# Kernel optimization log

Hardware: AMD Instinct MI355X
Metric: run time of the kernel (lower is better)

Reference implementation:

```python
import jax, jax.numpy as jnp
import numpy as np

D = 128  # time-encoder dimension == attention embed_dim


def harmonic_encode(ts, basis_freq):
    # ts: (N,) -> (N, D); phases are zero in the original module
    m = ts[:, None] * basis_freq[None, :]
    return jnp.sqrt(1.0 / D) * jnp.concatenate([jnp.cos(m), jnp.sin(m)], axis=1)


def mha_1head(q, k, mask, Wq, bq, Wk, bk, Wv, bv, Wo, bo):
    # Single-head nn.MultiheadAttention. q: (T, D) queries (torch batch dim),
    # k: (S, D) shared keys/values (original repeats these T times; same math),
    # mask: (T, S) True = masked out (key_padding_mask semantics).
    qp = q @ Wq.T + bq
    kp = k @ Wk.T + bk
    vp = k @ Wv.T + bv
    scores = jnp.einsum('td,sd->ts', qp, kp) / jnp.sqrt(jnp.asarray(D, q.dtype))
    scores = jnp.where(mask, -jnp.inf, scores)
    attn = jax.nn.softmax(scores, axis=-1)  # (T, S)
    return (attn @ vp) @ Wo.T + bo


def setup_inputs() -> dict:
    key = jax.random.key(0)
    ks = jax.random.split(key, 24)
    T, L, V = 4096, 8192, 1000
    s = 1.0 / np.sqrt(D)
    inp = {
        't': jax.random.uniform(ks[0], (T,), jnp.float32),
        'e_nodes_ts': jax.random.uniform(ks[1], (L,), jnp.float32),
        'e_nodes_exp': jax.random.randint(ks[2], (L,), 0, V),
        'e_node_target': jax.random.randint(ks[3], (1,), 0, V),
        'basis_freq': jnp.asarray(1.0 / 5.0 ** np.linspace(1, 9, D // 2), jnp.float32),
        'phi': jnp.ones((1,), jnp.float32),
        'W_lin': jax.random.normal(ks[4], (1, 2 * D), jnp.float32) * 0.05,
        'b_lin': jnp.zeros((1,), jnp.float32),
    }
    kidx = 5
    for suf in ('_s', '_n'):
        for nm in ('Wq', 'Wk', 'Wv', 'Wo'):
            inp[nm + suf] = jax.random.normal(ks[kidx], (D, D), jnp.float32) * s
            kidx += 1
        for nm in ('bq', 'bk', 'bv', 'bo'):
            inp[nm + suf] = jnp.zeros((D,), jnp.float32)
    return inp


def reference(t, e_nodes_ts, e_nodes_exp, e_node_target, basis_freq, phi, W_lin, b_lin,
              Wq_s, Wk_s, Wv_s, Wo_s, bq_s, bk_s, bv_s, bo_s,
              Wq_n, Wk_n, Wv_n, Wo_n, bq_n, bk_n, bv_n, bo_n):
    # prepend sentinels exactly as the torch forward does
    ts_all = jnp.concatenate([jnp.zeros((2,), e_nodes_ts.dtype), e_nodes_ts])      # (S,)
    exp_all = jnp.concatenate([jnp.full((1,), -1, e_nodes_exp.dtype), e_node_target, e_nodes_exp])  # (S,)

    phi_t = harmonic_encode(t, basis_freq)        # (T, D)
    phi_ts = harmonic_encode(ts_all, basis_freq)  # (S, D)

    pad = ts_all[None, :] > t[:, None]            # (T, S) future events masked
    self_mask = pad | (exp_all != e_node_target[0])[None, :]
    neig_mask = pad | (exp_all == e_node_target[0])[None, :]

    out_s = mha_1head(phi_t, phi_ts, self_mask, Wq_s, bq_s, Wk_s, bk_s, Wv_s, bv_s, Wo_s, bo_s)
    out_n = mha_1head(phi_t, phi_ts, neig_mask, Wq_n, bq_n, Wk_n, bk_n, Wv_n, bv_n, Wo_n, bo_n)
    atten_output = jnp.concatenate([out_s, out_n], axis=1)  # (T, 2D)

    lam = atten_output @ W_lin.T + b_lin          # (T, 1)
    x = lam * phi
    x = jnp.where(x > 20.0, 20.0, x)              # clamp as in soft_plus()
    lambdav = (1.0 / phi) * jnp.log1p(jnp.exp(x))
    return lambdav, atten_output
```

## Files before the change

### kernel.cpp

```cpp
#include <hip/hip_runtime.h>

#define T_Q 4096
#define S_TOT 8194
#define S_ALLOC 8256
#define SELF_CAP 128
#define NSEG 23
#define NSLOT 24
#define NCH64 129
#define SCALE 0.08838834764831843f
#define NEG_BIG -1.0e30f
#define TS_INF 3.0e38f

typedef __attribute__((ext_vector_type(8))) short short8;
typedef __attribute__((ext_vector_type(4))) float f32x4;
typedef __attribute__((ext_vector_type(4))) unsigned short ush4;
typedef unsigned short ush;
typedef unsigned int uint32;
typedef unsigned long long u64;

static __device__ __forceinline__ ush f2bf(float f) {
    unsigned int u = __float_as_uint(f);
    u += 0x7FFFu + ((u >> 16) & 1u);
    return (ush)(u >> 16);
}
static __device__ __forceinline__ float bf2f(ush u) {
    return __uint_as_float(((unsigned int)u) << 16);
}

__global__ __launch_bounds__(256) void prep_kernel(
    const float* __restrict__ t, const float* __restrict__ ets,
    const int* __restrict__ exps, const int* __restrict__ tgtp,
    const float* __restrict__ bf,
    const float* __restrict__ Wo_s, const float* __restrict__ Wv_s, const float* __restrict__ bv_s,
    const float* __restrict__ Wo_n, const float* __restrict__ Wv_n, const float* __restrict__ bv_n,
    const float* __restrict__ Wq_s, const float* __restrict__ Wq_n,
    const float* __restrict__ Wk_s, const float* __restrict__ Wk_n,
    ush* __restrict__ phi_t, ush* __restrict__ phi_ts,
    float* __restrict__ ts_pad, float* __restrict__ ts1, int* __restrict__ perm1,
    u64* __restrict__ maskbits, ush* __restrict__ Wb, float* __restrict__ bvo)
{
    __shared__ __align__(16) ush es[8192];
    __shared__ int swcnt[4];
    __shared__ int stot;
    float* red = (float*)es;
    int bid = blockIdx.x, tid = threadIdx.x;

    if (bid < 3088) {
        int R = bid * 4 + (tid >> 6);
        int j = tid & 63;
        float x; ush* dst;
        if (R < T_Q) { x = t[R]; dst = phi_t + (size_t)R * 128; }
        else {
            int s = R - T_Q;
            x = (s < 2) ? 0.0f : ((s < S_TOT) ? ets[s - 2] : 0.0f);
            dst = phi_ts + (size_t)s * 128;
        }
        float m = x * bf[j];
        dst[j]      = f2bf(__cosf(m) * SCALE);
        dst[64 + j] = f2bf(__sinf(m) * SCALE);
    } else if (bid == 3088) {
        int tgt = tgtp[0];
        for (int i = tid * 4; i < S_TOT - 2; i += 1024) {
            int4 v = *(const int4*)(exps + i);
            es[i] = (ush)v.x; es[i + 1] = (ush)v.y; es[i + 2] = (ush)v.z; es[i + 3] = (ush)v.w;
        }
        for (int i = tid; i < S_ALLOC; i += 256)
            ts_pad[i] = (i < 2) ? 0.f : ((i < S_TOT) ? ets[i - 2] : TS_INF);
        __syncthreads();
        ush tgt16 = (ush)tgt;
        int w4 = tid >> 6, lane = tid & 63;
        int cbeg = w4 * 33, cend = (w4 == 3) ? NCH64 : (cbeg + 33);
        u64 ltm = ((u64)1 << lane) - 1ull;
        int cnt = 0;
        for (int ch = cbeg; ch < cend; ++ch) {
            int s = ch * 64 + lane;
            bool m = (s < S_TOT) && ((s == 1) || (s >= 2 && es[s - 2] == tgt16));
            u64 b = __ballot(m);
            if (lane == 0) maskbits[ch] = b;
            cnt += __popcll(b);
        }
        if (lane == 0) swcnt[w4] = cnt;
        __syncthreads();
        if (tid == 0) {
            int a = 0;
            #pragma unroll
            for (int i = 0; i < 4; ++i) { int tc = swcnt[i]; swcnt[i] = a; a += tc; }
            stot = a;
        }
        __syncthreads();
        int off2 = swcnt[w4];
        for (int ch = cbeg; ch < cend; ++ch) {
            int s = ch * 64 + lane;
            bool m = (s < S_TOT) && ((s == 1) || (s >= 2 && es[s - 2] == tgt16));
            u64 b = __ballot(m);
            if (m) {
                int p = off2 + __popcll(b & ltm);
                if (p < SELF_CAP) { perm1[p] = s; ts1[p] = (s >= 2) ? ets[s - 2] : 0.f; }
            }
            off2 += __popcll(b);
        }
        __syncthreads();
        int st = stot > SELF_CAP ? SELF_CAP : stot;
        for (int i = st + tid; i < SELF_CAP; i += 256) { perm1[i] = 0; ts1[i] = TS_INF; }
    } else if (bid < 3217) {
        int row = bid - 3089;
        int h = tid >> 7, col = tid & 127;
        const float* Wo = h ? Wo_n : Wo_s;
        const float* Wv = h ? Wv_n : Wv_s;
        const float* bv = h ? bv_n : bv_s;
        float acc = 0.f;
        #pragma unroll 8
        for (int jj = 0; jj < 128; ++jj) acc += Wo[row * 128 + jj] * Wv[jj * 128 + col];
        Wb[(size_t)(4 + h) * 16384 + row * 128 + col] = f2bf(acc);
        red[tid] = Wo[row * 128 + col] * bv[col];
        __syncthreads();
        for (int off = 64; off > 0; off >>= 1) {
            if ((tid & 127) < off) red[tid] += red[tid + off];
            __syncthreads();
        }
        if ((tid & 127) == 0) bvo[h * 128 + row] = red[tid];
    } else {
        int idx = (bid - 3217) * 256 + tid;
        int which = idx >> 14, e = idx & 16383;
        const float* src;
        switch (which) {
            case 0: src = Wq_s; break; case 1: src = Wq_n; break;
            case 2: src = Wk_s; break; default: src = Wk_n; break;
        }
        Wb[idx] = f2bf(src[e]);
    }
}

__global__ __launch_bounds__(256) void proj_kernel(
    const ush* __restrict__ phi_t, const ush* __restrict__ phi_ts, const ush* __restrict__ Wb,
    const float* __restrict__ bq_s, const float* __restrict__ bq_n,
    const float* __restrict__ bk_s, const float* __restrict__ bk_n,
    const float* __restrict__ bvo, const int* __restrict__ perm1,
    ush* __restrict__ qp, ush* __restrict__ kpc, ush* __restrict__ vpoT)
{
    int y = blockIdx.y;
    const float* b; int M; const int* perm = nullptr; int ldv = 0;
    const ush* in = phi_ts;
    ush* out = nullptr; ush* outT = nullptr;
    switch (y) {
        case 0: b = bq_s;      M = T_Q; in = phi_t; out = qp; break;
        case 1: b = bq_n;      M = T_Q; in = phi_t; out = qp + (size_t)T_Q * 128; break;
        case 2: b = bk_s;      M = SELF_CAP; perm = perm1; out = kpc; break;
        case 3: b = bk_n;      M = S_ALLOC;  out = kpc + (size_t)SELF_CAP * 128; break;
        case 4: b = bvo;       M = SELF_CAP; perm = perm1; outT = vpoT; ldv = SELF_CAP; break;
        default:b = bvo + 128; M = S_ALLOC;  outT = vpoT + (size_t)SELF_CAP * 128; ldv = S_ALLOC; break;
    }
    int mbase = blockIdx.x * 64 + (int)(threadIdx.x >> 6) * 16;
    if (mbase >= M) return;
    int lane = threadIdx.x & 63, u = lane >> 4, c = lane & 15;
    const ush* arow = perm ? (in + (size_t)perm[mbase + c] * 128)
                           : (in + (size_t)(mbase + c) * 128);
    short8 af[4];
    #pragma unroll
    for (int ks = 0; ks < 4; ++ks) af[ks] = *(const short8*)(arow + ks * 32 + u * 8);
    const ush* W = Wb + (size_t)y * 16384;
    #pragma unroll
    for (int nt = 0; nt < 8; ++nt) {
        int ncol = nt * 16 + c;
        float bval = b[ncol];
        f32x4 acc = {bval, bval, bval, bval};
        #pragma unroll
        for (int ks = 0; ks < 4; ++ks) {
            short8 bf8 = *(const short8*)(W + ncol * 128 + ks * 32 + u * 8);
            acc = __builtin_amdgcn_mfma_f32_16x16x32_bf16(af[ks], bf8, acc, 0, 0, 0);
        }
        if (outT) {
            ush4 pk;
            #pragma unroll
            for (int r = 0; r < 4; ++r) pk[r] = f2bf(acc[r]);
            *(ush4*)(outT + (size_t)ncol * ldv + mbase + u * 4) = pk;
        } else {
            #pragma unroll
            for (int r = 0; r < 4; ++r)
                out[(size_t)(mbase + u * 4 + r) * 128 + ncol] = f2bf(acc[r]);
        }
    }
}

__global__ __launch_bounds__(256, 2) void attn_kernel(
    const ush* __restrict__ qp, const ush* __restrict__ kpc, const ush* __restrict__ vpoT,
    const float* __restrict__ ts_pad, const float* __restrict__ ts1,
    const u64* __restrict__ maskbits, const float* __restrict__ tq,
    ush* __restrict__ Opart, float* __restrict__ mpart, float* __restrict__ lpart)
{
    int bid = ((int)blockIdx.x & 7) * 96 + ((int)blockIdx.x >> 3);
    int head, qb, slot, t0, t1;
    if (bid < 32 * NSEG) {
        head = 1; int seg = bid >> 5; qb = bid & 31; slot = seg;
        t0 = seg * NCH64 / NSEG; t1 = (seg + 1) * NCH64 / NSEG;
    } else {
        head = 0; qb = bid - 32 * NSEG; slot = NSEG; t0 = 0; t1 = SELF_CAP / 64;
    }
    const ush* kph = kpc  + (head ? (size_t)SELF_CAP * 128 : 0);
    const ush* vph = vpoT + (head ? (size_t)SELF_CAP * 128 : 0);
    const int ld = head ? S_ALLOC : SELF_CAP;
    const float* tsh = head ? ts_pad : ts1;
    const ush* qph = qp + (head ? (size_t)T_Q * 128 : 0);

    __shared__ __align__(16) ush K2[2][64 * 128];
    __shared__ __align__(16) ush V1[128 * 64];
    __shared__ float tsb[2][64];

    int tid = threadIdx.x, w = tid >> 6, lane = tid & 63;
    int u = lane >> 4, c = lane & 15;
    int qrow0 = qb * 128 + w * 32;
    int sbase = (lane & 48) + ((lane & 48) >> 2);

    short8 qf[2][4];
    #pragma unroll
    for (int qg = 0; qg < 2; ++qg) {
        const ush* qr = qph + (size_t)(qrow0 + qg * 16 + c) * 128;
        #pragma unroll
        for (int ks = 0; ks < 4; ++ks) qf[qg][ks] = *(const short8*)(qr + ks * 32 + u * 8);
    }
    float t_c[2] = { tq[qrow0 + c], tq[qrow0 + 16 + c] };

    f32x4 Ov[2][8];
    #pragma unroll
    for (int qg = 0; qg < 2; ++qg)
        #pragma unroll
        for (int dt = 0; dt < 8; ++dt) Ov[qg][dt] = (f32x4){0.f, 0.f, 0.f, 0.f};
    float mrow[2] = {NEG_BIG, NEG_BIG}, lrow[2] = {0.f, 0.f};

    short8 kreg[4], vreg[4]; float tsreg = 0.f;
    int kr = tid >> 2, kq = tid & 3;
    int vd = tid >> 1, vh = tid & 1;

    auto LOADT = [&](int t) {
        int kb = t * 64;
        const ush* src = kph + (size_t)(kb + kr) * 128 + kq * 32;
        #pragma unroll
        for (int i = 0; i < 4; ++i) kreg[i] = *(const short8*)(src + i * 8);
        const ush* vsrc = vph + (size_t)vd * ld + kb + vh * 32;
        #pragma unroll
        for (int i = 0; i < 4; ++i) vreg[i] = *(const short8*)(vsrc + i * 8);
        if (tid < 64) tsreg = tsh[kb + tid];
    };
    auto WRITE_K = [&](int b) {
        #pragma unroll
        for (int i = 0; i < 4; ++i)
            *(short8*)&K2[b][kr * 128 + (((kq * 4 + i) ^ (kr & 7)) << 3)] = kreg[i];
        if (tid < 64) tsb[b][tid] = tsreg;
    };
    auto WRITE_V = [&]() {
        #pragma unroll
        for (int i = 0; i < 4; ++i)
            *(short8*)&V1[vd * 64 + (((vh * 4 + i) ^ (vd & 7)) << 3)] = vreg[i];
    };

    LOADT(t0); WRITE_K(0); WRITE_V();
    __syncthreads();

    for (int t = t0; t < t1; ++t) {
        int cur = (t - t0) & 1;
        bool pre = (t + 1 < t1);
        u64 mk = head ? maskbits[t] : 0ull;
        if (pre) LOADT(t + 1);

        float sc[2][4][4];
        #pragma unroll
        for (int ct = 0; ct < 4; ++ct) {
            short8 kf[4];
            int row = ct * 16 + c;
            #pragma unroll
            for (int ks = 0; ks < 4; ++ks)
                kf[ks] = *(const short8*)&K2[cur][row * 128 + (((ks * 4 + u) ^ (row & 7)) << 3)];
            f32x4 acc0 = {0.f, 0.f, 0.f, 0.f}, acc1 = {0.f, 0.f, 0.f, 0.f};
            #pragma unroll
            for (int ks = 0; ks < 4; ++ks) {
                acc0 = __builtin_amdgcn_mfma_f32_16x16x32_bf16(kf[ks], qf[0][ks], acc0, 0, 0, 0);
                acc1 = __builtin_amdgcn_mfma_f32_16x16x32_bf16(kf[ks], qf[1][ks], acc1, 0, 0, 0);
            }
            f32x4 ts4 = *(const f32x4*)&tsb[cur][ct * 16 + u * 4];
            uint32 mh = (uint32)(mk >> (ct * 16 + u * 4));
            #pragma unroll
            for (int r = 0; r < 4; ++r) {
                bool em = (mh >> r) & 1u;
                sc[0][ct][r] = (em || ts4[r] > t_c[0]) ? NEG_BIG : acc0[r] * SCALE;
                sc[1][ct][r] = (em || ts4[r] > t_c[1]) ? NEG_BIG : acc1[r] * SCALE;
            }
        }
        if (pre) WRITE_K(cur ^ 1);

        short8 pfq[2][2];
        #pragma unroll
        for (int qg = 0; qg < 2; ++qg) {
            float mt = sc[qg][0][0];
            #pragma unroll
            for (int ct = 0; ct < 4; ++ct)
                #pragma unroll
                for (int r = 0; r < 4; ++r) mt = fmaxf(mt, sc[qg][ct][r]);
            mt = fmaxf(mt, __shfl_xor(mt, 16));
            mt = fmaxf(mt, __shfl_xor(mt, 32));
            if (__any(mt > mrow[qg])) {
                float mnew = fmaxf(mrow[qg], mt);
                float sf = __expf(mrow[qg] - mnew);
                mrow[qg] = mnew;
                lrow[qg] *= sf;
                float sfr[4];
                #pragma unroll
                for (int r = 0; r < 4; ++r) sfr[r] = __shfl(sf, sbase + r);
                #pragma unroll
                for (int dt = 0; dt < 8; ++dt) {
                    Ov[qg][dt][0] *= sfr[0]; Ov[qg][dt][1] *= sfr[1];
                    Ov[qg][dt][2] *= sfr[2]; Ov[qg][dt][3] *= sfr[3];
                }
            }
            float p[4][4], s16 = 0.f;
            #pragma unroll
            for (int ct = 0; ct < 4; ++ct)
                #pragma unroll
                for (int r = 0; r < 4; ++r) { p[ct][r] = __expf(sc[qg][ct][r] - mrow[qg]); s16 += p[ct][r]; }
            s16 += __shfl_xor(s16, 16);
            s16 += __shfl_xor(s16, 32);
            lrow[qg] += s16;

            uint32 q0[4], q1[4];
            #pragma unroll
            for (int ct = 0; ct < 4; ++ct) {
                asm("v_cvt_pk_bf16_f32 %0, %1, %2" : "=v"(q0[ct]) : "v"(p[ct][0]), "v"(p[ct][1]));
                asm("v_cvt_pk_bf16_f32 %0, %1, %2" : "=v"(q1[ct]) : "v"(p[ct][2]), "v"(p[ct][3]));
            }
            #pragma unroll
            for (int ksl = 0; ksl < 2; ++ksl) {
                uint32 a0 = q0[2 * ksl], b0 = q0[2 * ksl + 1];
                uint32 a1 = q1[2 * ksl], b1 = q1[2 * ksl + 1];
                asm("v_permlane32_swap_b32 %0, %1" : "+v"(a0), "+v"(b0));
                asm("v_permlane16_swap_b32 %0, %1" : "+v"(a0), "+v"(b0));
                asm("v_permlane32_swap_b32 %0, %1" : "+v"(a1), "+v"(b1));
                asm("v_permlane16_swap_b32 %0, %1" : "+v"(a1), "+v"(b1));
                union { uint32 w4[4]; short8 s8; } pk_;
                pk_.w4[0] = a0; pk_.w4[1] = a1; pk_.w4[2] = b0; pk_.w4[3] = b1;
                pfq[qg][ksl] = pk_.s8;
            }
        }

        #pragma unroll
        for (int ksl = 0; ksl < 2; ++ksl)
            #pragma unroll
            for (int dt = 0; dt < 8; ++dt) {
                int d = dt * 16 + c;
                short8 vf = *(const short8*)&V1[d * 64 + (((ksl * 4 + u) ^ (d & 7)) << 3)];
                Ov[0][dt] = __builtin_amdgcn_mfma_f32_16x16x32_bf16(pfq[0][ksl], vf, Ov[0][dt], 0, 0, 0);
                Ov[1][dt] = __builtin_amdgcn_mfma_f32_16x16x32_bf16(pfq[1][ksl], vf, Ov[1][dt], 0, 0, 0);
            }

        __syncthreads();
        if (pre) WRITE_V();
        __syncthreads();
    }

    size_t rbase = (size_t)slot * T_Q + qrow0;
    #pragma unroll
    for (int qg = 0; qg < 2; ++qg)
        #pragma unroll
        for (int dt = 0; dt < 8; ++dt)
            #pragma unroll
            for (int r = 0; r < 4; ++r)
                Opart[(rbase + qg * 16 + u * 4 + r) * 128 + dt * 16 + c] = f2bf(Ov[qg][dt][r]);
    if (u == 0) {
        mpart[rbase + c] = mrow[0];      lpart[rbase + c] = lrow[0];
        mpart[rbase + 16 + c] = mrow[1]; lpart[rbase + 16 + c] = lrow[1];
    }
}

__global__ __launch_bounds__(256) void combine_kernel(
    const ush* __restrict__ Opart, const float* __restrict__ mpart, const float* __restrict__ lpart,
    const float* __restrict__ bo_s, const float* __restrict__ bo_n,
    const float* __restrict__ Wl, const float* __restrict__ bl,
    const float* __restrict__ phi, float* __restrict__ outp)
{
    int row = blockIdx.x, tid = threadIdx.x;
    float outv;
    if (tid < 128) {
        size_t rb = (size_t)NSEG * T_Q + row;
        outv = bf2f(Opart[rb * 128 + tid]) / lpart[rb] + bo_s[tid];
    } else {
        int d = tid - 128;
        float M = NEG_BIG;
        #pragma unroll
        for (int z = 0; z < NSEG; ++z) M = fmaxf(M, mpart[(size_t)z * T_Q + row]);
        float L = 0.f, O = 0.f;
        #pragma unroll
        for (int z = 0; z < NSEG; ++z) {
            size_t rb = (size_t)z * T_Q + row;
            float wz = __expf(mpart[rb] - M);
            L += wz * lpart[rb];
            O += wz * bf2f(Opart[rb * 128 + d]);
        }
        outv = O / L + bo_n[d];
    }
    outp[T_Q + (size_t)row * 256 + tid] = outv;

    float dot = outv * Wl[tid];
    #pragma unroll
    for (int off = 1; off < 64; off <<= 1) dot += __shfl_xor(dot, off);
    __shared__ float wsum[4];
    if ((tid & 63) == 0) wsum[tid >> 6] = dot;
    __syncthreads();
    if (tid == 0) {
        float s = wsum[0] + wsum[1] + wsum[2] + wsum[3];
        float ph = phi[0];
        float x = (s + bl[0]) * ph;
        x = fminf(x, 20.0f);
        outp[row] = log1pf(__expf(x)) / ph;
    }
}

extern "C" void kernel_launch(void* const* d_in, const int* in_sizes, int n_in,
                              void* d_out, int out_size, void* d_ws, size_t ws_size,
                              hipStream_t stream) {
    (void)in_sizes; (void)n_in; (void)out_size; (void)ws_size;
    const float* t    = (const float*)d_in[0];
    const float* ets  = (const float*)d_in[1];
    const int*   exps = (const int*)d_in[2];
    const int*   tgt  = (const int*)d_in[3];
    const float* bfq  = (const float*)d_in[4];
    const float* phi  = (const float*)d_in[5];
    const float* Wlin = (const float*)d_in[6];
    const float* blin = (const float*)d_in[7];
    const float* Wq_s = (const float*)d_in[8];
    const float* Wk_s = (const float*)d_in[9];
    const float* Wv_s = (const float*)d_in[10];
    const float* Wo_s = (const float*)d_in[11];
    const float* bq_s = (const float*)d_in[12];
    const float* bk_s = (const float*)d_in[13];
    const float* bv_s = (const float*)d_in[14];
    const float* bo_s = (const float*)d_in[15];
    const float* Wq_n = (const float*)d_in[16];
    const float* Wk_n = (const float*)d_in[17];
    const float* Wv_n = (const float*)d_in[18];
    const float* Wo_n = (const float*)d_in[19];
    const float* bq_n = (const float*)d_in[20];
    const float* bk_n = (const float*)d_in[21];
    const float* bv_n = (const float*)d_in[22];
    const float* bo_n = (const float*)d_in[23];

    char* ws = (char*)d_ws;
    size_t off = 0;
    auto alloc = [&](size_t bytes) { void* p = ws + off; off += (bytes + 255) & ~(size_t)255; return p; };
    ush* phi_t  = (ush*)alloc((size_t)T_Q * 128 * 2);
    ush* phi_ts = (ush*)alloc((size_t)S_ALLOC * 128 * 2);
    ush* qpb    = (ush*)alloc((size_t)2 * T_Q * 128 * 2);
    ush* kpc    = (ush*)alloc((size_t)(SELF_CAP + S_ALLOC) * 128 * 2);
    ush* vpoT   = (ush*)alloc((size_t)128 * (SELF_CAP + S_ALLOC) * 2);
    int*    perm1 = (int*)   alloc((size_t)SELF_CAP * 4);
    float*  ts1   = (float*) alloc((size_t)SELF_CAP * 4);
    float*  ts_pad= (float*) alloc((size_t)S_ALLOC * 4);
    u64*    maskb = (u64*)   alloc((size_t)NCH64 * 8);
    float*  bvo   = (float*) alloc((size_t)2 * 128 * 4);
    ush*    Wb    = (ush*)   alloc((size_t)6 * 16384 * 2);
    ush*    Opart = (ush*)   alloc((size_t)NSLOT * T_Q * 128 * 2);
    float*  mpart = (float*) alloc((size_t)NSLOT * T_Q * 4);
    float*  lpart = (float*) alloc((size_t)NSLOT * T_Q * 4);

    float* outp = (float*)d_out;

    prep_kernel<<<dim3(3473), dim3(256), 0, stream>>>(
        t, ets, exps, tgt, bfq, Wo_s, Wv_s, bv_s, Wo_n, Wv_n, bv_n,
        Wq_s, Wq_n, Wk_s, Wk_n, phi_t, phi_ts, ts_pad, ts1, perm1, maskb, Wb, bvo);
    proj_kernel<<<dim3(129, 6), dim3(256), 0, stream>>>(
        phi_t, phi_ts, Wb, bq_s, bq_n, bk_s, bk_n, bvo, perm1, qpb, kpc, vpoT);
    attn_kernel<<<dim3(32 * NSEG + 32), dim3(256), 0, stream>>>(
        qpb, kpc, vpoT, ts_pad, ts1, maskb, t, Opart, mpart, lpart);
    combine_kernel<<<dim3(T_Q), dim3(256), 0, stream>>>(
        Opart, mpart, lpart, bo_s, bo_n, Wlin, blin, phi, outp);
}
```

Measured before the change: 95.55 us.

## Software-pipeline QK^T one tile ahead with double-buffered K and V

Restructures the attention loop so the QK^T scores for tile t+1 are computed while softmax and PV for tile t run, letting MFMA work from both stages interleave. V is now double-buffered in shared memory and written with K in one step, and global loads are issued two tiles ahead. This is meant to hide the latency of the softmax and exp chain and of the global loads. In exchange it doubles V's shared-memory footprint and keeps two score arrays live in registers, which may reduce occupancy or cause spills.

```diff
diff --git a/kernel.cpp b/kernel.cpp
--- a/kernel.cpp
+++ b/kernel.cpp
@@ -203,7 +203,7 @@
     const ush* qph = qp + (head ? (size_t)T_Q * 128 : 0);
 
     __shared__ __align__(16) ush K2[2][64 * 128];
-    __shared__ __align__(16) ush V1[128 * 64];
+    __shared__ __align__(16) ush V2[2][128 * 64];
     __shared__ float tsb[2][64];
 
     int tid = threadIdx.x, w = tid >> 6, lane = tid & 63;
@@ -241,42 +241,33 @@
         for (int i = 0; i < 4; ++i) vreg[i] = *(const short8*)(vsrc + i * 8);
         if (tid < 64) tsreg = tsh[kb + tid];
     };
-    auto WRITE_K = [&](int b) {
+    auto WRITE_KV = [&](int b) {
         #pragma unroll
         for (int i = 0; i < 4; ++i)
             *(short8*)&K2[b][kr * 128 + (((kq * 4 + i) ^ (kr & 7)) << 3)] = kreg[i];
+        #pragma unroll
+        for (int i = 0; i < 4; ++i)
+            *(short8*)&V2[b][vd * 64 + (((vh * 4 + i) ^ (vd & 7)) << 3)] = vreg[i];
         if (tid < 64) tsb[b][tid] = tsreg;
     };
-    auto WRITE_V = [&]() {
-        #pragma unroll
-        for (int i = 0; i < 4; ++i)
-            *(short8*)&V1[vd * 64 + (((vh * 4 + i) ^ (vd & 7)) << 3)] = vreg[i];
-    };
-
-    LOADT(t0); WRITE_K(0); WRITE_V();
-    __syncthreads();
-
-    for (int t = t0; t < t1; ++t) {
-        int cur = (t - t0) & 1;
-        bool pre = (t + 1 < t1);
-        u64 mk = head ? maskbits[t] : 0ull;
-        if (pre) LOADT(t + 1);
-
-        float sc[2][4][4];
+
+    float scA[2][4][4], scB[2][4][4];
+    auto QKT = [&](int buf, int tt, float (*sc)[4][4]) {
+        u64 mk = head ? maskbits[tt] : 0ull;
         #pragma unroll
         for (int ct = 0; ct < 4; ++ct) {
             short8 kf[4];
             int row = ct * 16 + c;
             #pragma unroll
             for (int ks = 0; ks < 4; ++ks)
-                kf[ks] = *(const short8*)&K2[cur][row * 128 + (((ks * 4 + u) ^ (row & 7)) << 3)];
+                kf[ks] = *(const short8*)&K2[buf][row * 128 + (((ks * 4 + u) ^ (row & 7)) << 3)];
             f32x4 acc0 = {0.f, 0.f, 0.f, 0.f}, acc1 = {0.f, 0.f, 0.f, 0.f};
             #pragma unroll
             for (int ks = 0; ks < 4; ++ks) {
                 acc0 = __builtin_amdgcn_mfma_f32_16x16x32_bf16(kf[ks], qf[0][ks], acc0, 0, 0, 0);
                 acc1 = __builtin_amdgcn_mfma_f32_16x16x32_bf16(kf[ks], qf[1][ks], acc1, 0, 0, 0);
             }
-            f32x4 ts4 = *(const f32x4*)&tsb[cur][ct * 16 + u * 4];
+            f32x4 ts4 = *(const f32x4*)&tsb[buf][ct * 16 + u * 4];
             uint32 mh = (uint32)(mk >> (ct * 16 + u * 4));
             #pragma unroll
             for (int r = 0; r < 4; ++r) {
@@ -285,16 +276,28 @@
                 sc[1][ct][r] = (em || ts4[r] > t_c[1]) ? NEG_BIG : acc1[r] * SCALE;
             }
         }
-        if (pre) WRITE_K(cur ^ 1);
+    };
+
+    LOADT(t0); WRITE_KV(0);
+    __syncthreads();
+    if (t0 + 1 < t1) LOADT(t0 + 1);
+    QKT(0, t0, scA);
+    if (t0 + 1 < t1) WRITE_KV(1);
+    __syncthreads();
+    if (t0 + 2 < t1) LOADT(t0 + 2);
+
+    for (int t = t0; t < t1; ++t) {
+        int cur = (t - t0) & 1;
+        if (t + 1 < t1) QKT(cur ^ 1, t + 1, scB);
 
         short8 pfq[2][2];
         #pragma unroll
         for (int qg = 0; qg < 2; ++qg) {
-            float mt = sc[qg][0][0];
+            float mt = scA[qg][0][0];
             #pragma unroll
             for (int ct = 0; ct < 4; ++ct)
                 #pragma unroll
-                for (int r = 0; r < 4; ++r) mt = fmaxf(mt, sc[qg][ct][r]);
+                for (int r = 0; r < 4; ++r) mt = fmaxf(mt, scA[qg][ct][r]);
             mt = fmaxf(mt, __shfl_xor(mt, 16));
             mt = fmaxf(mt, __shfl_xor(mt, 32));
             if (__any(mt > mrow[qg])) {
@@ -315,7 +318,7 @@
             #pragma unroll
             for (int ct = 0; ct < 4; ++ct)
                 #pragma unroll
-                for (int r = 0; r < 4; ++r) { p[ct][r] = __expf(sc[qg][ct][r] - mrow[qg]); s16 += p[ct][r]; }
+                for (int r = 0; r < 4; ++r) { p[ct][r] = __expf(scA[qg][ct][r] - mrow[qg]); s16 += p[ct][r]; }
             s16 += __shfl_xor(s16, 16);
             s16 += __shfl_xor(s16, 32);
             lrow[qg] += s16;
@@ -345,14 +348,22 @@
             #pragma unroll
             for (int dt = 0; dt < 8; ++dt) {
                 int d = dt * 16 + c;
-                short8 vf = *(const short8*)&V1[d * 64 + (((ksl * 4 + u) ^ (d & 7)) << 3)];
+                short8 vf = *(const short8*)&V2[cur][d * 64 + (((ksl * 4 + u) ^ (d & 7)) << 3)];
                 Ov[0][dt] = __builtin_amdgcn_mfma_f32_16x16x32_bf16(pfq[0][ksl], vf, Ov[0][dt], 0, 0, 0);
                 Ov[1][dt] = __builtin_amdgcn_mfma_f32_16x16x32_bf16(pfq[1][ksl], vf, Ov[1][dt], 0, 0, 0);
             }
 
         __syncthreads();
-        if (pre) WRITE_V();
-        __syncthreads();
+        if (t + 2 < t1) WRITE_KV(cur);
+        __syncthreads();
+        if (t + 3 < t1) LOADT(t + 3);
+
+        #pragma unroll
+        for (int qg = 0; qg < 2; ++qg)
+            #pragma unroll
+            for (int ct = 0; ct < 4; ++ct)
+                #pragma unroll
+                for (int r = 0; r < 4; ++r) scA[qg][ct][r] = scB[qg][ct][r];
     }
 
     size_t rbase = (size_t)slot * T_Q + qrow0;
```

After: 99.22 us. +3.8%, slower.
